# Performance work log

Hardware: AMD Instinct MI355X
Metric: run time of the kernel (lower is better)

The kernel has to match this reference:

```python
import jax, jax.numpy as jnp
import numpy as np

EPS = 1e-5
B, CIN, L = 512, 5, 1024   # batch, input channels, msp length == d_model
COUT, A, NB = 32, 13, 5    # CNN branch channels, max_atoms, num_bonds_prediction


def conv1d(x, w, pad, groups=1):
    # x: (N, C, L), w: (O, I/groups, K)
    return jax.lax.conv_general_dilated(
        x, w, window_strides=(1,), padding=[(pad, pad)],
        dimension_numbers=("NCH", "OIH", "NCH"), feature_group_count=groups)


def batchnorm(x, g, b):
    # training-mode BN over (N, L) per channel, as nn.BatchNorm1d in train()
    m = jnp.mean(x, axis=(0, 2), keepdims=True)
    v = jnp.var(x, axis=(0, 2), keepdims=True)
    return (x - m) * jax.lax.rsqrt(v + EPS) * g[None, :, None] + b[None, :, None]


def setup_inputs() -> dict:
    key = jax.random.key(0)
    ks = jax.random.split(key, 16)
    n = jax.random.normal
    inp = {
        "src": n(ks[0], (B, CIN, L), dtype=jnp.float32),
        "mask": jnp.ones((B, A), dtype=bool),
        "max_atoms": A,
        # CNN branch 1 (kernel 5) : depthwise, pointwise, BN, residual 1x1 conv
        "dw1": n(ks[1], (CIN, 1, 5), dtype=jnp.float32) * 0.2,
        "pw1": n(ks[2], (COUT, CIN, 1), dtype=jnp.float32) * 0.2,
        "g1": jnp.ones((COUT,), jnp.float32),
        "be1": jnp.zeros((COUT,), jnp.float32),
        "r1w": n(ks[3], (COUT, CIN, 1), dtype=jnp.float32) * 0.2,
        "r1b": jnp.zeros((COUT,), jnp.float32),
        # CNN branch 2 (kernel 3)
        "dw2": n(ks[4], (CIN, 1, 3), dtype=jnp.float32) * 0.2,
        "pw2": n(ks[5], (COUT, CIN, 1), dtype=jnp.float32) * 0.2,
        "g2": jnp.ones((COUT,), jnp.float32),
        "be2": jnp.zeros((COUT,), jnp.float32),
        "r2w": n(ks[6], (COUT, CIN, 1), dtype=jnp.float32) * 0.2,
        "r2b": jnp.zeros((COUT,), jnp.float32),
        # EdgeClassify2 linears: ll1 (2*COUT -> A), fl (2*L -> NB)
        "ll1w": n(ks[7], (A, 2 * COUT), dtype=jnp.float32) * 0.1,
        "ll1b": jnp.zeros((A,), jnp.float32),
        "flw": n(ks[8], (NB, 2 * L), dtype=jnp.float32) * 0.02,
        "flb": jnp.zeros((NB,), jnp.float32),
    }
    return inp


def reference(src, mask, max_atoms, dw1, pw1, g1, be1, r1w, r1b,
              dw2, pw2, g2, be2, r2w, r2b, ll1w, ll1b, flw, flb):
    # ---- CNN encoder ----
    e1 = jax.nn.relu(batchnorm(conv1d(conv1d(src, dw1, 2, groups=CIN), pw1, 0), g1, be1))
    e1 = e1 * (conv1d(src, r1w, 0) + r1b[None, :, None])
    e2 = jax.nn.relu(batchnorm(conv1d(conv1d(src, dw2, 1, groups=CIN), pw2, 0), g2, be2))
    e2 = e2 * (conv1d(src, r2w, 0) + r2b[None, :, None])
    x = jnp.concatenate([e1, e2], axis=1)          # (B, 2*COUT, L)
    # ---- EdgeClassify2 ----
    # ll1 over channel dim: (B, 2*COUT, L) -> (B, A, L)
    h = jnp.einsum("bcl,ac->bal", x, ll1w) + ll1b[None, :, None]
    # vectorized replacement of the O(A^2) python loop:
    # final_e[:, i, j] = concat(h[:, min(i,j)], h[:, max(i,j)])
    idx = jnp.arange(max_atoms)
    mn = jnp.minimum(idx[:, None], idx[None, :])   # (A, A)
    mx = jnp.maximum(idx[:, None], idx[None, :])
    final_e = jnp.concatenate([h[:, mn, :], h[:, mx, :]], axis=-1)  # (B, A, A, 2L)
    out = jnp.einsum("bijd,nd->bijn", final_e, flw) + flb           # (B, A, A, NB)
    return out
```

## Files before the change

### kernel.cpp

```cpp
#include <hip/hip_runtime.h>
#include <hip/hip_bf16.h>

#define BB 512
#define LL 1024
#define AA 13
#define NBP 5
#define NTOT (BB * LL)
#define EPSV 1e-5f

#define WS_F     192
#define WS_PART  256
#define WS_CONST 10496
#define WS_FLW   16384

typedef __attribute__((ext_vector_type(8))) short bhalf8;
typedef __attribute__((ext_vector_type(4))) float floatx4;

__device__ __forceinline__ void trunc_pair(float e0, float e1, unsigned int& hp, unsigned int& lp) {
    unsigned int u0 = __float_as_uint(e0), u1 = __float_as_uint(e1);
    unsigned int h0 = u0 & 0xFFFF0000u, h1 = u1 & 0xFFFF0000u;
    hp = (h0 >> 16) | h1;
    float l0 = e0 - __uint_as_float(h0);
    float l1 = e1 - __uint_as_float(h1);
    lp = (__float_as_uint(l0) >> 16) | (__float_as_uint(l1) & 0xFFFF0000u);
}

template<int CTRL, int RM, bool BC>
__device__ __forceinline__ float dppadd(float v) {
    int t = __builtin_amdgcn_update_dpp(0, __float_as_int(v), CTRL, RM, 0xf, BC);
    return v + __int_as_float(t);
}
__device__ __forceinline__ float wave_sum(float v) {
    v = dppadd<0x111, 0xf, true >(v);
    v = dppadd<0x112, 0xf, true >(v);
    v = dppadd<0x114, 0xf, true >(v);
    v = dppadd<0x118, 0xf, true >(v);
    v = dppadd<0x142, 0xa, false>(v);
    v = dppadd<0x143, 0xc, false>(v);
    return v;
}

__global__ __launch_bounds__(256) void k_moments(
    const float* __restrict__ src,
    const float* __restrict__ dw1,
    const float* __restrict__ dw2,
    const float* __restrict__ flw,
    float* __restrict__ ws)
{
    __shared__ float red[4][40];
    __shared__ float fred[4];
    int tid = threadIdx.x;
    int gid = blockIdx.x * 256 + tid;
    int b = gid >> 7, L0 = (gid & 127) << 3;
    const float* sb = src + b * (5 * LL);

    float w1[5][5], w2[5][3];
#pragma unroll
    for (int c = 0; c < 5; c++) {
#pragma unroll
        for (int t = 0; t < 5; t++) w1[c][t] = dw1[c*5+t];
#pragma unroll
        for (int t = 0; t < 3; t++) w2[c][t] = dw2[c*3+t];
    }

    float x[5][16];
#pragma unroll
    for (int c5 = 0; c5 < 5; c5++) {
        const float* sp = sb + c5 * LL;
        float4 xa = (L0 >= 4)    ? *(const float4*)(sp + L0 - 4) : make_float4(0,0,0,0);
        float4 xb = *(const float4*)(sp + L0);
        float4 xc = *(const float4*)(sp + L0 + 4);
        float4 xd = (L0 <= 1012) ? *(const float4*)(sp + L0 + 8) : make_float4(0,0,0,0);
        x[c5][0]=xa.x; x[c5][1]=xa.y; x[c5][2]=xa.z; x[c5][3]=xa.w;
        x[c5][4]=xb.x; x[c5][5]=xb.y; x[c5][6]=xb.z; x[c5][7]=xb.w;
        x[c5][8]=xc.x; x[c5][9]=xc.y; x[c5][10]=xc.z; x[c5][11]=xc.w;
        x[c5][12]=xd.x; x[c5][13]=xd.y; x[c5][14]=xd.z; x[c5][15]=xd.w;
    }

    float acc[40];
#pragma unroll
    for (int k = 0; k < 40; k++) acc[k] = 0.f;

#pragma unroll
    for (int k = 0; k < 8; k++) {
        float d1[5], d2[5];
#pragma unroll
        for (int c5 = 0; c5 < 5; c5++) {
            d1[c5] = w1[c5][0]*x[c5][k+2] + w1[c5][1]*x[c5][k+3] + w1[c5][2]*x[c5][k+4]
                   + w1[c5][3]*x[c5][k+5] + w1[c5][4]*x[c5][k+6];
            d2[c5] = w2[c5][0]*x[c5][k+3] + w2[c5][1]*x[c5][k+4] + w2[c5][2]*x[c5][k+5];
        }
#pragma unroll
        for (int j = 0; j < 5; j++) { acc[j] += d1[j]; acc[20+j] += d2[j]; }
#pragma unroll
        for (int j = 0; j < 5; j++)
#pragma unroll
            for (int kk = j; kk < 5; kk++) {
                int idx = j*(11-j)/2 + (kk - j);
                acc[5+idx]  += d1[j]*d1[kk];
                acc[25+idx] += d2[j]*d2[kk];
            }
    }

    int lane = tid & 63, wv = tid >> 6;
#pragma unroll
    for (int k = 0; k < 40; k++) acc[k] = wave_sum(acc[k]);
    if (lane == 63) {
#pragma unroll
        for (int k = 0; k < 40; k++) red[wv][k] = acc[k];
    }
    __syncthreads();
    if (tid < 40) {
        ws[WS_PART + blockIdx.x * 40 + tid] =
            red[0][tid] + red[1][tid] + red[2][tid] + red[3][tid];
    }

    if (blockIdx.x < 10) {
        int nn = blockIdx.x;
        int n = nn < 5 ? nn : nn - 5;
        int off = nn < 5 ? 0 : LL;
        float4 v = *(const float4*)(flw + n * (2*LL) + off + tid * 4);
        {
            unsigned int hp0, lp0, hp1, lp1;
            trunc_pair(v.x, v.y, hp0, lp0);
            trunc_pair(v.z, v.w, hp1, lp1);
            char* fwb = (char*)(ws + WS_FLW);
            *(uint2*)(fwb + nn * 2048 + tid * 8)         = make_uint2(hp0, hp1);
            *(uint2*)(fwb + 32768 + nn * 2048 + tid * 8) = make_uint2(lp0, lp1);
        }
        float s = wave_sum(v.x + v.y + v.z + v.w);
        if (lane == 63) fred[wv] = s;
        __syncthreads();
        if (tid == 0) ws[WS_F + nn] = fred[0] + fred[1] + fred[2] + fred[3];
    } else if (blockIdx.x < 16) {
        int nn = blockIdx.x;
        char* fwb = (char*)(ws + WS_FLW);
        *(uint2*)(fwb + nn * 2048 + tid * 8)         = make_uint2(0u, 0u);
        *(uint2*)(fwb + 32768 + nn * 2048 + tid * 8) = make_uint2(0u, 0u);
    }
}

__global__ __launch_bounds__(320) void k_prep(
    float* __restrict__ ws,
    const float* __restrict__ pw1, const float* __restrict__ pw2,
    const float* __restrict__ g1,  const float* __restrict__ be1,
    const float* __restrict__ g2,  const float* __restrict__ be2,
    const float* __restrict__ r1w, const float* __restrict__ r2w,
    const float* __restrict__ r1b, const float* __restrict__ r2b)
{
    __shared__ float momS[40];
    int tid = threadIdx.x;
    {
        int k = tid >> 3, sub = tid & 7;
        float v = 0.f;
#pragma unroll 8
        for (int t2 = 0; t2 < 32; t2++) v += ws[WS_PART + (sub + (t2 << 3)) * 40 + k];
        v += __shfl_xor(v, 1, 64);
        v += __shfl_xor(v, 2, 64);
        v += __shfl_xor(v, 4, 64);
        if (sub == 0) momS[k] = v;
    }
    __syncthreads();
    if (tid < 64) {
        int brc = tid >> 5, o = tid & 31;
        const float invN = 1.0f / (float)NTOT;
        const float* pw = brc ? pw2 : pw1;
        const float* rw = brc ? r2w : r1w;
        const float* s  = momS + (brc ? 20 : 0);
        const float* M  = momS + (brc ? 25 : 5);
        float pwv[5], rwv[5], md[5];
#pragma unroll
        for (int j = 0; j < 5; j++) { pwv[j] = pw[o*5+j]; rwv[j] = rw[o*5+j]; md[j] = s[j] * invN; }
        float meanY = 0.f;
#pragma unroll
        for (int j = 0; j < 5; j++) meanY += pwv[j] * md[j];
        float ey2 = 0.f;
#pragma unroll
        for (int j = 0; j < 5; j++)
#pragma unroll
            for (int k = 0; k < 5; k++) {
                int lo = j < k ? j : k, hi = j < k ? k : j;
                int idx = lo*(11-lo)/2 + (hi - lo);
                ey2 += pwv[j] * pwv[k] * (M[idx] * invN);
            }
        float varY = ey2 - meanY * meanY;
        if (varY < 0.f) varY = 0.f;
        float gg = brc ? g2[o] : g1[o];
        float bb = brc ? be2[o] : be1[o];
        float rb = brc ? r2b[o] : r1b[o];
        float sc = gg * rsqrtf(varY + EPSV);
        float sh = bb - meanY * sc;
        float* dst = ws + WS_CONST + tid * 16;
        dst[0] = pwv[0]*sc; dst[1] = pwv[1]*sc; dst[2] = pwv[2]*sc; dst[3] = pwv[3]*sc;
        dst[4] = pwv[4]*sc; dst[5] = sh;        dst[6] = rb;        dst[7] = 0.f;
        dst[8] = rwv[0];    dst[9] = rwv[1];    dst[10] = rwv[2];   dst[11] = rwv[3];
        dst[12] = rwv[4];   dst[13] = 0.f;      dst[14] = 0.f;      dst[15] = 0.f;
    }
}

__global__ __launch_bounds__(512, 2) void k_fused(
    const float* __restrict__ src,
    const float* __restrict__ dw1,
    const float* __restrict__ dw2,
    const float* __restrict__ ll1w,
    const float* __restrict__ ll1b,
    const float* __restrict__ flb,
    const float* __restrict__ ws_ro,
    float* __restrict__ out)
{
    __shared__ __align__(16) float dvS[18432];
    __shared__ float llT[832];
    __shared__ float PQ[130];

    int tid = threadIdx.x, b = blockIdx.x;
    int lane = tid & 63;
    int gu = __builtin_amdgcn_readfirstlane(tid >> 6);
    int mt = gu & 3, lq = gu >> 2;
    int br = mt >> 1;

    const float* srcB = src + b * (5 * LL);
    char* base  = (char*)dvS;
    char* cbase = (char*)(dvS + 16384);

    for (int t = tid; t < 1024; t += 512) {
        int swz = ((t >> 3) & 3) << 4;
        float d1v[5], d2v[5], s0[5];
#pragma unroll
        for (int c5 = 0; c5 < 5; c5++) {
            const float* s5 = srcB + (c5 << 10);
            float xm2 = (t >= 2)    ? s5[t - 2] : 0.f;
            float xm1 = (t >= 1)    ? s5[t - 1] : 0.f;
            float x0  = s5[t];
            float xp1 = (t <= 1022) ? s5[t + 1] : 0.f;
            float xp2 = (t <= 1021) ? s5[t + 2] : 0.f;
            d1v[c5] = dw1[c5*5+0]*xm2 + dw1[c5*5+1]*xm1 + dw1[c5*5+2]*x0
                    + dw1[c5*5+3]*xp1 + dw1[c5*5+4]*xp2;
            d2v[c5] = dw2[c5*3+0]*xm1 + dw2[c5*3+1]*x0 + dw2[c5*3+2]*xp1;
            s0[c5] = x0;
        }
        *(float4*)(base + ((((0<<11)+(t<<1)+0) << 4) ^ swz)) = make_float4(d1v[0],d1v[1],d1v[2],d1v[3]);
        *(float4*)(base + ((((0<<11)+(t<<1)+1) << 4) ^ swz)) = make_float4(d1v[4],s0[0],s0[1],s0[2]);
        *(float4*)(base + ((((1<<11)+(t<<1)+0) << 4) ^ swz)) = make_float4(d2v[0],d2v[1],d2v[2],d2v[3]);
        *(float4*)(base + ((((1<<11)+(t<<1)+1) << 4) ^ swz)) = make_float4(d2v[4],s0[0],s0[1],s0[2]);
        *(float2*)(cbase + (t << 3)) = make_float2(s0[3], s0[4]);
    }
    for (int idx = tid; idx < 832; idx += 512) {
        int cc = idx / 13, a = idx - cc * 13;
        llT[idx] = ll1w[a * 64 + cc];
    }
    __syncthreads();

    int ch = (mt << 4) + (lane & 15);
    const float* cf = ws_ro + WS_CONST + (ch << 4);
    const float4 A  = *(const float4*)cf;
    const float4 B2 = *(const float4*)(cf + 4);
    const float4 R0 = *(const float4*)(cf + 8);
    const float r4w = cf[12];

    int nB = lane & 15;
    int kg = (lane >> 4) << 3;
    const char* fwb = (const char*)(ws_ro + WS_FLW);
    floatx4 Cacc = {0.f, 0.f, 0.f, 0.f};

#pragma unroll 1
    for (int s = 0; s < 16; ++s) {
        int lb = (lq << 9) + (s << 5) + kg;
        union { uint4 u; bhalf8 v; } bh, bl;
        bh.u = *(const uint4*)(fwb + (((nB << 10) + lb) << 1));
        bl.u = *(const uint4*)(fwb + 32768 + (((nB << 10) + lb) << 1));
        int sw = ((lb >> 3) & 3) << 4;
        float e[8];
#pragma unroll
        for (int i = 0; i < 8; ++i) {
            int l = lb + i;
            const float4 pa = *(const float4*)(base + ((((br<<11)+(l<<1)+0) << 4) ^ sw));
            const float4 pb = *(const float4*)(base + ((((br<<11)+(l<<1)+1) << 4) ^ sw));
            const float2 pc = *(const float2*)(cbase + (l << 3));
            float y = B2.y + A.x*pa.x + A.y*pa.y + A.z*pa.z + A.w*pa.w + B2.x*pb.x;
            float r = B2.z + R0.x*pb.y + R0.y*pb.z + R0.z*pb.w + R0.w*pc.x + r4w*pc.y;
            e[i] = fmaxf(y, 0.f) * r;
        }
        union { unsigned int u[4]; bhalf8 v; } ah, al;
#pragma unroll
        for (int j = 0; j < 4; j++) trunc_pair(e[2*j], e[2*j+1], ah.u[j], al.u[j]);
        Cacc = __builtin_amdgcn_mfma_f32_16x16x32_bf16(ah.v, bh.v, Cacc, 0, 0, 0);
        Cacc = __builtin_amdgcn_mfma_f32_16x16x32_bf16(ah.v, bl.v, Cacc, 0, 0, 0);
        Cacc = __builtin_amdgcn_mfma_f32_16x16x32_bf16(al.v, bh.v, Cacc, 0, 0, 0);
    }

    __syncthreads();
    {
        float* part = dvS;
        int basep = (gu << 8) + ((lane >> 4) << 6) + (lane & 15);
        part[basep]      = Cacc[0];
        part[basep + 16] = Cacc[1];
        part[basep + 32] = Cacc[2];
        part[basep + 48] = Cacc[3];
    }
    __syncthreads();
    float* SarrF = dvS + 4096;
    for (int idx = tid; idx < 1024; idx += 512) {
        int c = idx >> 4, n = idx & 15;
        int mt2 = c >> 4, m = c & 15;
        const float* part = (const float*)dvS;
        int o = (m << 4) + n;
        SarrF[idx] = part[mt2 * 256 + o] + part[(4 + mt2) * 256 + o];
    }
    __syncthreads();

    if (tid < 130) {
        int half = tid >= 65 ? 1 : 0;
        int q = tid - half * 65;
        int a = q / 5, n = q - a * 5;
        int col = half * 5 + n;
        float v = ll1b[a] * ws_ro[WS_F + col];
#pragma unroll 8
        for (int cc = 0; cc < 64; cc++) v += llT[cc * 13 + a] * SarrF[(cc << 4) + col];
        PQ[tid] = v;
    }
    __syncthreads();

    for (int idx = tid; idx < AA * AA * NBP; idx += 512) {
        int i = idx / 65;
        int rr = idx - i * 65;
        int j = rr / 5, n = rr - j * 5;
        int mn = i < j ? i : j, mx = i < j ? j : i;
        out[b * (AA * AA * NBP) + idx] = PQ[mn * 5 + n] + PQ[65 + mx * 5 + n] + flb[n];
    }
}

extern "C" void kernel_launch(void* const* d_in, const int* in_sizes, int n_in,
                              void* d_out, int out_size, void* d_ws, size_t ws_size,
                              hipStream_t stream) {
    const float* src  = (const float*)d_in[0];
    const float* dw1  = (const float*)d_in[3];
    const float* pw1  = (const float*)d_in[4];
    const float* g1   = (const float*)d_in[5];
    const float* be1  = (const float*)d_in[6];
    const float* r1w  = (const float*)d_in[7];
    const float* r1b  = (const float*)d_in[8];
    const float* dw2  = (const float*)d_in[9];
    const float* pw2  = (const float*)d_in[10];
    const float* g2   = (const float*)d_in[11];
    const float* be2  = (const float*)d_in[12];
    const float* r2w  = (const float*)d_in[13];
    const float* r2b  = (const float*)d_in[14];
    const float* ll1w = (const float*)d_in[15];
    const float* ll1b = (const float*)d_in[16];
    const float* flw  = (const float*)d_in[17];
    const float* flb  = (const float*)d_in[18];
    float* ws  = (float*)d_ws;
    float* out = (float*)d_out;

    k_moments<<<256, 256, 0, stream>>>(src, dw1, dw2, flw, ws);
    k_prep<<<1, 320, 0, stream>>>(ws, pw1, pw2, g1, be1, g2, be2, r1w, r2w, r1b, r2b);
    k_fused<<<BB, 512, 0, stream>>>(src, dw1, dw2, ll1w, ll1b, flb, ws, out);
}
```

Measured before the change: 134.1 us.

## Compute two channel tiles per wave to reuse LDS loads and B fragments

Each wave now handles two 16-channel M tiles (32 channels) over a quarter of the sequence, instead of one tile over half of it. The shared-memory activation loads and the global B-fragment loads are reused for both tiles, which cuts LDS traffic per MFMA. The per-wave loop runs 8 K steps instead of 16. In exchange the cross-wave reduction becomes a 4-way sum instead of 2-way, and register pressure goes up because two sets of per-channel constants and two accumulators are live.

```diff
diff --git a/kernel.cpp b/kernel.cpp
--- a/kernel.cpp
+++ b/kernel.cpp
@@ -198,6 +198,13 @@
     }
 }
 
+__device__ __forceinline__ float e_val(const float4& A, const float4& B2, const float4& R0, float r4w,
+                                       const float4& pa, const float4& pb, float svx, float svy) {
+    float y = B2.y + A.x*pa.x + A.y*pa.y + A.z*pa.z + A.w*pa.w + B2.x*pb.x;
+    float r = B2.z + R0.x*pb.y + R0.y*pb.z + R0.z*pb.w + R0.w*svx + r4w*svy;
+    return fmaxf(y, 0.f) * r;
+}
+
 __global__ __launch_bounds__(512, 2) void k_fused(
     const float* __restrict__ src,
     const float* __restrict__ dw1,
@@ -215,8 +222,10 @@
     int tid = threadIdx.x, b = blockIdx.x;
     int lane = tid & 63;
     int gu = __builtin_amdgcn_readfirstlane(tid >> 6);
-    int mt = gu & 3, lq = gu >> 2;
-    int br = mt >> 1;
+    int mp = gu >> 2;
+    int lq = gu & 3;
+    int row = lane & 15;
+    int ko = lane >> 4;
 
     const float* srcB = src + b * (5 * LL);
     char* base  = (char*)dvS;
@@ -250,61 +259,86 @@
     }
     __syncthreads();
 
-    int ch = (mt << 4) + (lane & 15);
-    const float* cf = ws_ro + WS_CONST + (ch << 4);
-    const float4 A  = *(const float4*)cf;
-    const float4 B2 = *(const float4*)(cf + 4);
-    const float4 R0 = *(const float4*)(cf + 8);
-    const float r4w = cf[12];
-
-    int nB = lane & 15;
-    int kg = (lane >> 4) << 3;
+    int chA = (mp << 5) + row;
+    int chB = chA + 16;
+    const float* cfA = ws_ro + WS_CONST + (chA << 4);
+    const float4 Aa = *(const float4*)cfA;
+    const float4 Ba = *(const float4*)(cfA + 4);
+    const float4 Ra = *(const float4*)(cfA + 8);
+    const float  a4 = cfA[12];
+    const float* cfB = ws_ro + WS_CONST + (chB << 4);
+    const float4 Ab = *(const float4*)cfB;
+    const float4 Bb = *(const float4*)(cfB + 4);
+    const float4 Rb = *(const float4*)(cfB + 8);
+    const float  b4 = cfB[12];
+
     const char* fwb = (const char*)(ws_ro + WS_FLW);
-    floatx4 Cacc = {0.f, 0.f, 0.f, 0.f};
+    floatx4 CA = {0.f, 0.f, 0.f, 0.f};
+    floatx4 CB = {0.f, 0.f, 0.f, 0.f};
 
 #pragma unroll 1
-    for (int s = 0; s < 16; ++s) {
-        int lb = (lq << 9) + (s << 5) + kg;
+    for (int s = 0; s < 8; ++s) {
+        int kstep = (lq << 3) + s;
+        int l0 = (kstep << 5) + (ko << 3);
         union { uint4 u; bhalf8 v; } bh, bl;
-        bh.u = *(const uint4*)(fwb + (((nB << 10) + lb) << 1));
-        bl.u = *(const uint4*)(fwb + 32768 + (((nB << 10) + lb) << 1));
-        int sw = ((lb >> 3) & 3) << 4;
-        float e[8];
-#pragma unroll
-        for (int i = 0; i < 8; ++i) {
-            int l = lb + i;
-            const float4 pa = *(const float4*)(base + ((((br<<11)+(l<<1)+0) << 4) ^ sw));
-            const float4 pb = *(const float4*)(base + ((((br<<11)+(l<<1)+1) << 4) ^ sw));
-            const float2 pc = *(const float2*)(cbase + (l << 3));
-            float y = B2.y + A.x*pa.x + A.y*pa.y + A.z*pa.z + A.w*pa.w + B2.x*pb.x;
-            float r = B2.z + R0.x*pb.y + R0.y*pb.z + R0.z*pb.w + R0.w*pc.x + r4w*pc.y;
-            e[i] = fmaxf(y, 0.f) * r;
-        }
-        union { unsigned int u[4]; bhalf8 v; } ah, al;
-#pragma unroll
-        for (int j = 0; j < 4; j++) trunc_pair(e[2*j], e[2*j+1], ah.u[j], al.u[j]);
-        Cacc = __builtin_amdgcn_mfma_f32_16x16x32_bf16(ah.v, bh.v, Cacc, 0, 0, 0);
-        Cacc = __builtin_amdgcn_mfma_f32_16x16x32_bf16(ah.v, bl.v, Cacc, 0, 0, 0);
-        Cacc = __builtin_amdgcn_mfma_f32_16x16x32_bf16(al.v, bh.v, Cacc, 0, 0, 0);
+        {
+            int boff = ((row << 10) + l0) << 1;
+            bh.u = *(const uint4*)(fwb + boff);
+            bl.u = *(const uint4*)(fwb + 32768 + boff);
+        }
+        int sw = ((l0 >> 3) & 3) << 4;
+        int ebase = (mp << 15) + (l0 << 5);
+        union { unsigned int u[4]; bhalf8 v; } ahA, alA, ahB, alB;
+#pragma unroll
+        for (int jp = 0; jp < 4; ++jp) {
+            int o0 = ebase + (jp << 6);
+            const float4 pa0 = *(const float4*)(base + ((o0      ) ^ sw));
+            const float4 pb0 = *(const float4*)(base + ((o0 + 16) ^ sw));
+            const float4 pa1 = *(const float4*)(base + ((o0 + 32) ^ sw));
+            const float4 pb1 = *(const float4*)(base + ((o0 + 48) ^ sw));
+            const float4 pcc = *(const float4*)(cbase + ((l0 + (jp << 1)) << 3));
+            float e0 = e_val(Aa, Ba, Ra, a4, pa0, pb0, pcc.x, pcc.y);
+            float e1 = e_val(Aa, Ba, Ra, a4, pa1, pb1, pcc.z, pcc.w);
+            trunc_pair(e0, e1, ahA.u[jp], alA.u[jp]);
+            float f0 = e_val(Ab, Bb, Rb, b4, pa0, pb0, pcc.x, pcc.y);
+            float f1 = e_val(Ab, Bb, Rb, b4, pa1, pb1, pcc.z, pcc.w);
+            trunc_pair(f0, f1, ahB.u[jp], alB.u[jp]);
+        }
+        CA = __builtin_amdgcn_mfma_f32_16x16x32_bf16(ahA.v, bh.v, CA, 0, 0, 0);
+        CA = __builtin_amdgcn_mfma_f32_16x16x32_bf16(ahA.v, bl.v, CA, 0, 0, 0);
+        CA = __builtin_amdgcn_mfma_f32_16x16x32_bf16(alA.v, bh.v, CA, 0, 0, 0);
+        CB = __builtin_amdgcn_mfma_f32_16x16x32_bf16(ahB.v, bh.v, CB, 0, 0, 0);
+        CB = __builtin_amdgcn_mfma_f32_16x16x32_bf16(ahB.v, bl.v, CB, 0, 0, 0);
+        CB = __builtin_amdgcn_mfma_f32_16x16x32_bf16(alB.v, bh.v, CB, 0, 0, 0);
     }
 
     __syncthreads();
     {
         float* part = dvS;
-        int basep = (gu << 8) + ((lane >> 4) << 6) + (lane & 15);
-        part[basep]      = Cacc[0];
-        part[basep + 16] = Cacc[1];
-        part[basep + 32] = Cacc[2];
-        part[basep + 48] = Cacc[3];
+        int basep = ((lane >> 4) << 6) + (lane & 15);
+        int sA = (gu << 1) * 256, sB = sA + 256;
+        part[sA + basep]      = CA[0];
+        part[sA + basep + 16] = CA[1];
+        part[sA + basep + 32] = CA[2];
+        part[sA + basep + 48] = CA[3];
+        part[sB + basep]      = CB[0];
+        part[sB + basep + 16] = CB[1];
+        part[sB + basep + 32] = CB[2];
+        part[sB + basep + 48] = CB[3];
     }
     __syncthreads();
     float* SarrF = dvS + 4096;
     for (int idx = tid; idx < 1024; idx += 512) {
         int c = idx >> 4, n = idx & 15;
         int mt2 = c >> 4, m = c & 15;
+        int mp2 = mt2 >> 1, t2 = mt2 & 1;
         const float* part = (const float*)dvS;
         int o = (m << 4) + n;
-        SarrF[idx] = part[mt2 * 256 + o] + part[(4 + mt2) * 256 + o];
+        float sum = 0.f;
+#pragma unroll
+        for (int lq2 = 0; lq2 < 4; ++lq2)
+            sum += part[((((mp2 << 2) + lq2) << 1) + t2) * 256 + o];
+        SarrF[idx] = sum;
     }
     __syncthreads();
 
```

After: 130.1 us. -3.0%, faster.
